# Performance work log

Measured on AMD Instinct MI355X. Metric: run time of the kernel, lower is better.

The kernel has to match this reference:

```python
import jax, jax.numpy as jnp
import numpy as np

D_HEAD = 64
IGNORE = -100000.0


def setup_inputs() -> dict:
    key = jax.random.key(0)
    ks = jax.random.split(key, 5)
    B, S, D, H, M = 2, 2048, 768, 12, D_HEAD
    scale = 0.05  # 'random_normal' keras init stddev
    return {
        "x": jax.random.normal(ks[0], (B, S, D), jnp.float32),
        "W_Q": jax.random.normal(ks[1], (H, D, M), jnp.float32) * scale,
        "b_Q": jnp.zeros((H, M), jnp.float32),
        "W_K": jax.random.normal(ks[2], (H, D, M), jnp.float32) * scale,
        "b_K": jnp.zeros((H, M), jnp.float32),
        "W_V": jax.random.normal(ks[3], (H, D, M), jnp.float32) * scale,
        "b_V": jnp.zeros((H, M), jnp.float32),
        "W_O": jax.random.normal(ks[4], (H, M, D), jnp.float32) * scale,
        "b_O": jnp.zeros((D,), jnp.float32),
    }


def reference(x, W_Q, b_Q, W_K, b_K, W_V, b_V, W_O, b_O):
    # q,k,v: [b, s, h, m]
    q = jnp.einsum("bqd,hdm->bqhm", x, W_Q) + b_Q
    k = jnp.einsum("bkd,hdm->bkhm", x, W_K) + b_K
    v = jnp.einsum("bkd,hdm->bkhm", x, W_V) + b_V
    # scores: [b, h, q, k], scaled by 1/sqrt(d_head)
    scores = jnp.einsum("bqhm,bkhm->bhqk", q, k) / jnp.sqrt(
        jnp.asarray(D_HEAD, q.dtype)
    )
    S = x.shape[1]
    # causal mask: strictly-upper-triangular positions set to IGNORE (-1e5),
    # matching tf.where(mask == 1, IGNORE, scores)
    causal = jnp.arange(S)[:, None] >= jnp.arange(S)[None, :]  # [q, k]
    scores = jnp.where(causal[None, None, :, :], scores, jnp.asarray(IGNORE, scores.dtype))
    pattern = jax.nn.softmax(scores, axis=-1)
    z = jnp.einsum("bhqk,bkhm->bqhm", pattern, v)
    attn_out = jnp.einsum("bqhm,hmd->bqd", z, W_O) + b_O
    return attn_out
```

## Files before the change

kernel.cpp:

```cpp
#include <hip/hip_runtime.h>
#include <hip/hip_bf16.h>
#include <cstdint>
#include <cstddef>

#define B_ 2
#define S_ 2048
#define D_ 768
#define H_ 12
#define M_ 64
#define BS_ (B_ * S_)
#define NQKV_ 2304
#define NCHUNK_ 80
#define TOTCHUNK_ (24 * NCHUNK_)
#define QSCALE 0.18033688011f

typedef __attribute__((ext_vector_type(8))) short bf16x8;
typedef __attribute__((ext_vector_type(4))) short bf16x4;
typedef __attribute__((ext_vector_type(4))) float f32x4;

__device__ __forceinline__ unsigned short f2bu(float f) {
    __hip_bfloat16 h = __float2bfloat16(f);
    unsigned short u;
    __builtin_memcpy(&u, &h, 2);
    return u;
}
__device__ __forceinline__ unsigned pack2(float a, float b) {
    return (unsigned)f2bu(a) | ((unsigned)f2bu(b) << 16);
}

__device__ __forceinline__ bf16x8 ld16(const unsigned short* p) {
    p = (const unsigned short*)__builtin_assume_aligned(p, 16);
    bf16x8 v; __builtin_memcpy(&v, p, 16); return v;
}
__device__ __forceinline__ bf16x4 ld8(const unsigned short* p) {
    p = (const unsigned short*)__builtin_assume_aligned(p, 8);
    bf16x4 v; __builtin_memcpy(&v, p, 8); return v;
}
__device__ __forceinline__ uint4 ld16u(const unsigned short* p) {
    p = (const unsigned short*)__builtin_assume_aligned(p, 16);
    uint4 v; __builtin_memcpy(&v, p, 16); return v;
}
__device__ __forceinline__ void st16(unsigned short* p, uint4 v) {
    p = (unsigned short*)__builtin_assume_aligned(p, 16);
    __builtin_memcpy(p, &v, 16);
}
__device__ __forceinline__ void st8(unsigned short* p, uint2 v) {
    p = (unsigned short*)__builtin_assume_aligned(p, 8);
    __builtin_memcpy(p, &v, 8);
}
__device__ __forceinline__ float4 ldf4(const float* p) {
    p = (const float*)__builtin_assume_aligned(p, 16);
    float4 v; __builtin_memcpy(&v, p, 16); return v;
}
__device__ __forceinline__ void async16(const unsigned short* g, unsigned short* l) {
    __builtin_amdgcn_global_load_lds(
        (const __attribute__((address_space(1))) void*)g,
        (__attribute__((address_space(3))) void*)l, 16, 0, 0);
}
__device__ __forceinline__ void b82f(uint4 u, float* o) {
    o[0] = __uint_as_float(u.x << 16); o[1] = __uint_as_float(u.x & 0xffff0000u);
    o[2] = __uint_as_float(u.y << 16); o[3] = __uint_as_float(u.y & 0xffff0000u);
    o[4] = __uint_as_float(u.z << 16); o[5] = __uint_as_float(u.z & 0xffff0000u);
    o[6] = __uint_as_float(u.w << 16); o[7] = __uint_as_float(u.w & 0xffff0000u);
}

#define NEG_BIG (-3.0e38f)

__global__ void prep(const float* __restrict__ WQ, const float* __restrict__ WK,
                     const float* __restrict__ WV, const float* __restrict__ WO,
                     const float* __restrict__ x,
                     unsigned short* __restrict__ WT,
                     unsigned short* __restrict__ WOT,
                     unsigned short* __restrict__ xb)
{
    const int bx = blockIdx.x;
    if (bx < 216) {
        const int xx = bx % 9, yy = bx / 9;
        const int c  = xx * 256 + threadIdx.x;
        const int k0 = yy * 32;
        const int which = c / D_;
        const int r = c - which * D_;
        const int h = r >> 6, m = r & 63;
        const float* Wsel = (which == 0) ? WQ : (which == 1) ? WK : WV;
        const float* src = Wsel + (size_t)h * D_ * M_ + m;
        unsigned short* dst = WT + (size_t)c * D_ + k0;
        for (int i = 0; i < 32; i += 8) {
            float wv[8];
#pragma unroll
            for (int j = 0; j < 8; j++) wv[j] = src[(size_t)(k0 + i + j) * M_];
            uint4 pu;
            pu.x = pack2(wv[0], wv[1]); pu.y = pack2(wv[2], wv[3]);
            pu.z = pack2(wv[4], wv[5]); pu.w = pack2(wv[6], wv[7]);
            st16(dst + i, pu);
        }
    } else if (bx < 288) {
        const int b2 = bx - 216;
        const int xx = b2 % 3, yy = b2 / 3;
        const int c  = xx * 256 + threadIdx.x;
        const int k0 = yy * 32;
        unsigned short* dst = WOT + (size_t)c * D_ + k0;
        for (int i = 0; i < 32; i += 8) {
            float wv[8];
#pragma unroll
            for (int j = 0; j < 8; j++) wv[j] = WO[(size_t)(k0 + i + j) * D_ + c];
            uint4 pu;
            pu.x = pack2(wv[0], wv[1]); pu.y = pack2(wv[2], wv[3]);
            pu.z = pack2(wv[4], wv[5]); pu.w = pack2(wv[6], wv[7]);
            st16(dst + i, pu);
        }
    } else {
        const size_t i = ((size_t)(bx - 288) * 256 + threadIdx.x) * 16;
#pragma unroll
        for (int p = 0; p < 2; p++) {
            float4 a0 = ldf4(x + i + p * 8), a1 = ldf4(x + i + p * 8 + 4);
            uint4 u;
            u.x = pack2(a0.x, a0.y); u.y = pack2(a0.z, a0.w);
            u.z = pack2(a1.x, a1.y); u.w = pack2(a1.z, a1.w);
            st16(xb + i + p * 8, u);
        }
    }
}

__global__ __launch_bounds__(256, 2) void qkv_gemm(
    const unsigned short* __restrict__ xb,
    const unsigned short* __restrict__ WT,
    const float* __restrict__ bQ, const float* __restrict__ bK,
    const float* __restrict__ bV,
    unsigned short* __restrict__ qo, unsigned short* __restrict__ ko,
    unsigned short* __restrict__ vt)
{
    const int row0 = blockIdx.x * 128;
    const int col0 = blockIdx.y * 128;
    const int t = threadIdx.x;
    const int w = t >> 6, lane = t & 63, quad = lane >> 4, l16 = lane & 15;
    const int wrow0 = (w & 1) * 64, wcol0 = (w >> 1) * 64;

    __shared__ unsigned short Alds[128 * 64];
    __shared__ unsigned short Blds[128 * 64];

    f32x4 acc[4][4] = {};

    const unsigned short* asrc[4];
    const unsigned short* bsrc[4];
    int ldsoff[4];
#pragma unroll
    for (int q = 0; q < 4; q++) {
        const int cq = w * 256 + q * 64 + lane;
        const int row = cq >> 3, c = cq & 7;
        const int cs = c ^ (row & 7);
        asrc[q] = xb + (size_t)(row0 + row) * D_ + cs * 8;
        bsrc[q] = WT + (size_t)(col0 + row) * D_ + cs * 8;
        ldsoff[q] = (w * 256 + q * 64) * 8;
    }
    const int swz = (l16 & 7);

    for (int k0 = 0; k0 < D_; k0 += 64) {
#pragma unroll
        for (int q = 0; q < 4; q++) async16(asrc[q] + k0, Alds + ldsoff[q]);
#pragma unroll
        for (int q = 0; q < 4; q++) async16(bsrc[q] + k0, Blds + ldsoff[q]);
        __syncthreads();

        bf16x8 af[4][2], bfm[4][2];
#pragma unroll
        for (int rt = 0; rt < 4; rt++) {
            const int row = wrow0 + rt * 16 + l16;
#pragma unroll
            for (int hh = 0; hh < 2; hh++)
                af[rt][hh] = ld16(&Alds[row * 64 + ((hh * 4 + quad) ^ swz) * 8]);
        }
#pragma unroll
        for (int st = 0; st < 4; st++) {
            const int row = wcol0 + st * 16 + l16;
#pragma unroll
            for (int hh = 0; hh < 2; hh++)
                bfm[st][hh] = ld16(&Blds[row * 64 + ((hh * 4 + quad) ^ swz) * 8]);
        }
#pragma unroll
        for (int rt = 0; rt < 4; rt++)
#pragma unroll
            for (int st = 0; st < 4; st++) {
                acc[rt][st] = __builtin_amdgcn_mfma_f32_16x16x32_bf16(
                    af[rt][0], bfm[st][0], acc[rt][st], 0, 0, 0);
                acc[rt][st] = __builtin_amdgcn_mfma_f32_16x16x32_bf16(
                    af[rt][1], bfm[st][1], acc[rt][st], 0, 0, 0);
            }
        __syncthreads();
    }

    const int which = col0 / D_;
    const int colin = col0 - which * D_;

    if (which < 2) {
        const float* bias = (which == 0) ? bQ : bK;
        unsigned short* outp = (which == 0) ? qo : ko;
        const float scale = (which == 0) ? QSCALE : 1.0f;
#pragma unroll
        for (int st = 0; st < 4; st++) {
            const int cl = colin + wcol0 + st * 16 + l16;
            const int h = cl >> 6, m = cl & 63;
            const float bval = bias[cl];
#pragma unroll
            for (int rt = 0; rt < 4; rt++)
#pragma unroll
                for (int rr = 0; rr < 4; rr++) {
                    const int R = row0 + wrow0 + rt * 16 + quad * 4 + rr;
                    const int bb = R >> 11, s = R & (S_ - 1);
                    outp[(((size_t)bb * H_ + h) * S_ + s) * M_ + m] =
                        f2bu((acc[rt][st][rr] + bval) * scale);
                }
        }
    } else {
#pragma unroll
        for (int st = 0; st < 4; st++) {
            const int cl = colin + wcol0 + st * 16 + l16;
            const int h = cl >> 6, m = cl & 63;
            const float bval = bV[cl];
#pragma unroll
            for (int rt = 0; rt < 4; rt++) {
                const int R0 = row0 + wrow0 + rt * 16 + quad * 4;
                const int bb = R0 >> 11, s0 = R0 & (S_ - 1);
                uint2 v;
                v.x = pack2(acc[rt][st][0] + bval, acc[rt][st][1] + bval);
                v.y = pack2(acc[rt][st][2] + bval, acc[rt][st][3] + bval);
                st8(&vt[(((size_t)bb * H_ + h) * M_ + m) * S_ + s0], v);
            }
        }
    }
}

struct StageRegs { uint4 ka[4]; uint4 va[4]; };

__device__ __forceinline__ void load_tile(const unsigned short* kb,
                                          const unsigned short* vb,
                                          int t, StageRegs& s)
{
#pragma unroll
    for (int q = 0; q < 4; q++) {
        const int ci = q * 256 + t;
        s.ka[q] = ld16u(kb + (size_t)(ci >> 3) * M_ + (ci & 7) * 8);
    }
#pragma unroll
    for (int q = 0; q < 4; q++) {
        const int ci = q * 256 + t;
        s.va[q] = ld16u(vb + (size_t)(ci >> 4) * S_ + (ci & 15) * 8);
    }
}

__global__ __launch_bounds__(256, 4) void attn_split(
    const unsigned short* __restrict__ Q,
    const unsigned short* __restrict__ Kin,
    const unsigned short* __restrict__ Vt,
    unsigned short* __restrict__ Opart,
    float* __restrict__ ml)
{
    const int xx = blockIdx.x;
    const int bh = blockIdx.y;

    int qt, c, nc;
    if (xx < 8)       { qt = xx; c = 0; nc = 1; }
    else if (xx < 24) { int u = xx - 8;  qt = 8  + (u >> 1); c = u & 1;  nc = 2; }
    else if (xx < 48) { int u = xx - 24; qt = 16 + u / 3;    c = u % 3;  nc = 3; }
    else              { int u = xx - 48; qt = 24 + (u >> 2); c = u & 3;  nc = 4; }

    const int ci     = bh * NCHUNK_ + xx;
    const int kbeg   = c * 512;
    const int keyend = min((qt + 1) * 64, kbeg + 512);
    const int iters  = (keyend - kbeg + 127) >> 7;
    const bool lastchunk = (c == nc - 1);

    const int t = threadIdx.x;
    const int wave = t >> 6, lane = t & 63, quad = lane >> 4, l16 = lane & 15;

    const unsigned short* Qb  = Q   + ((size_t)bh * S_ + qt * 64) * M_;
    const unsigned short* Kb  = Kin + (size_t)bh * S_ * M_;
    const unsigned short* VtB = Vt  + (size_t)bh * M_ * S_;

    __shared__ unsigned short Klds[128][72];
    __shared__ unsigned short Vlds[64][136];

    bf16x8 qf[2];
    {
        const unsigned short* qrow = Qb + (size_t)(wave * 16 + l16) * M_;
        qf[0] = ld16(qrow + quad * 8);
        qf[1] = ld16(qrow + 32 + quad * 8);
    }

    f32x4 o_acc[4] = {};
    float lrow = 0.f;

    StageRegs sr;
    load_tile(Kb + (size_t)kbeg * M_, VtB + kbeg, t, sr);

    for (int it = 0; it < iters; it++) {
        __syncthreads();
#pragma unroll
        for (int q = 0; q < 4; q++) {
            const int cq = q * 256 + t;
            st16(&Klds[cq >> 3][(cq & 7) * 8], sr.ka[q]);
        }
#pragma unroll
        for (int q = 0; q < 4; q++) {
            const int cq = q * 256 + t;
            st16(&Vlds[cq >> 4][(cq & 15) * 8], sr.va[q]);
        }
        __syncthreads();

        if (it + 1 < iters) {
            const int key1 = kbeg + (it + 1) * 128;
            load_tile(Kb + (size_t)key1 * M_, VtB + key1, t, sr);
        }

        f32x4 s_acc[8];
#pragma unroll
        for (int st = 0; st < 8; st++) {
            f32x4 z4 = {0.f, 0.f, 0.f, 0.f};
            bf16x8 kb0 = ld16(&Klds[st * 16 + l16][quad * 8]);
            bf16x8 kb1 = ld16(&Klds[st * 16 + l16][32 + quad * 8]);
            z4 = __builtin_amdgcn_mfma_f32_16x16x32_bf16(kb0, qf[0], z4, 0, 0, 0);
            z4 = __builtin_amdgcn_mfma_f32_16x16x32_bf16(kb1, qf[1], z4, 0, 0, 0);
            s_acc[st] = z4;
        }

        if (lastchunk && it == iters - 1) {
            const int keyq = kbeg + it * 128 + quad * 4;
            const int qg = qt * 64 + wave * 16 + l16;
#pragma unroll
            for (int st = 0; st < 8; st++)
#pragma unroll
                for (int r = 0; r < 4; r++)
                    if (keyq + st * 16 + r > qg)
                        s_acc[st][r] = -1e30f;
        }

        bf16x4 pkv[8];
#pragma unroll
        for (int st = 0; st < 8; st++) {
            float p0 = exp2f(s_acc[st][0]);
            float p1 = exp2f(s_acc[st][1]);
            float p2 = exp2f(s_acc[st][2]);
            float p3 = exp2f(s_acc[st][3]);
            lrow += (p0 + p1) + (p2 + p3);
            uint2 u;
            u.x = pack2(p0, p1);
            u.y = pack2(p2, p3);
            __builtin_memcpy(&pkv[st], &u, 8);
        }

#pragma unroll
        for (int stf = 0; stf < 4; stf++) {
#pragma unroll
            for (int st = 0; st < 8; st++) {
                bf16x4 va = ld8(&Vlds[stf * 16 + l16][st * 16 + quad * 4]);
                o_acc[stf] = __builtin_amdgcn_mfma_f32_16x16x16bf16_1k(
                    va, pkv[st], o_acc[stf], 0, 0, 0);
            }
        }
    }

    lrow += __shfl_xor(lrow, 16, 64);
    lrow += __shfl_xor(lrow, 32, 64);

    unsigned short* Op = Opart + (size_t)ci * 4096;
    const int q = wave * 16 + l16;
#pragma unroll
    for (int stf = 0; stf < 4; stf++) {
        uint2 u;
        u.x = pack2(o_acc[stf][0], o_acc[stf][1]);
        u.y = pack2(o_acc[stf][2], o_acc[stf][3]);
        st8(&Op[q * 64 + stf * 16 + quad * 4], u);
    }
    if (quad == 0)
        ml[(size_t)ci * 128 + 64 + q] = lrow;
}

__global__ void combine(const unsigned short* __restrict__ Opart,
                        const float* __restrict__ ml,
                        unsigned short* __restrict__ Z)
{
    const int qt = blockIdx.x, bh = blockIdx.y;
    const int b = bh / H_, h = bh - b * H_;
    const int g = qt >> 3, r7 = qt & 7;
    const int nc = g + 1;
    const int base = bh * NCHUNK_ + qt + 4 * g * (g - 1) + r7 * g;

    const int t = threadIdx.x;
    const int q = t >> 2, fs = (t & 3) * 16;

    float L = 0.f;
    for (int c = 0; c < nc; c++)
        L += ml[(size_t)(base + c) * 128 + 64 + q];
    const float invL = 1.0f / L;

    float o[16] = {};
    for (int c = 0; c < nc; c++) {
        const unsigned short* op =
            Opart + (size_t)(base + c) * 4096 + q * 64 + fs;
        float f[8];
        b82f(ld16u(op), f);
#pragma unroll
        for (int j = 0; j < 8; j++) o[j] += f[j];
        b82f(ld16u(op + 8), f);
#pragma unroll
        for (int j = 0; j < 8; j++) o[8 + j] += f[j];
    }

    unsigned short* zp =
        Z + ((size_t)b * S_ + qt * 64 + q) * (H_ * M_) + h * M_ + fs;
    uint4 u0, u1;
    u0.x = pack2(o[0]*invL,  o[1]*invL);  u0.y = pack2(o[2]*invL,  o[3]*invL);
    u0.z = pack2(o[4]*invL,  o[5]*invL);  u0.w = pack2(o[6]*invL,  o[7]*invL);
    u1.x = pack2(o[8]*invL,  o[9]*invL);  u1.y = pack2(o[10]*invL, o[11]*invL);
    u1.z = pack2(o[12]*invL, o[13]*invL); u1.w = pack2(o[14]*invL, o[15]*invL);
    st16(zp, u0);
    st16(zp + 8, u1);
}

__global__ __launch_bounds__(256, 2) void oproj_gemm(
    const unsigned short* __restrict__ Zin,
    const unsigned short* __restrict__ WOT,
    const float* __restrict__ bO,
    float* __restrict__ out)
{
    const int row0 = blockIdx.x * 128;
    const int col0 = blockIdx.y * 128;
    const int t = threadIdx.x;
    const int w = t >> 6, lane = t & 63, quad = lane >> 4, l16 = lane & 15;
    const int wrow0 = (w & 1) * 64, wcol0 = (w >> 1) * 64;

    __shared__ unsigned short Alds[128 * 64];
    __shared__ unsigned short Blds[128 * 64];

    f32x4 acc[4][4] = {};

    const unsigned short* asrc[4];
    const unsigned short* bsrc[4];
    int ldsoff[4];
#pragma unroll
    for (int q = 0; q < 4; q++) {
        const int cq = w * 256 + q * 64 + lane;
        const int row = cq >> 3, c = cq & 7;
        const int cs = c ^ (row & 7);
        asrc[q] = Zin + (size_t)(row0 + row) * D_ + cs * 8;
        bsrc[q] = WOT + (size_t)(col0 + row) * D_ + cs * 8;
        ldsoff[q] = (w * 256 + q * 64) * 8;
    }
    const int swz = (l16 & 7);

    for (int k0 = 0; k0 < D_; k0 += 64) {
#pragma unroll
        for (int q = 0; q < 4; q++) async16(asrc[q] + k0, Alds + ldsoff[q]);
#pragma unroll
        for (int q = 0; q < 4; q++) async16(bsrc[q] + k0, Blds + ldsoff[q]);
        __syncthreads();

        bf16x8 af[4][2], bfm[4][2];
#pragma unroll
        for (int rt = 0; rt < 4; rt++) {
            const int row = wrow0 + rt * 16 + l16;
#pragma unroll
            for (int hh = 0; hh < 2; hh++)
                af[rt][hh] = ld16(&Alds[row * 64 + ((hh * 4 + quad) ^ swz) * 8]);
        }
#pragma unroll
        for (int st = 0; st < 4; st++) {
            const int row = wcol0 + st * 16 + l16;
#pragma unroll
            for (int hh = 0; hh < 2; hh++)
                bfm[st][hh] = ld16(&Blds[row * 64 + ((hh * 4 + quad) ^ swz) * 8]);
        }
#pragma unroll
        for (int rt = 0; rt < 4; rt++)
#pragma unroll
            for (int st = 0; st < 4; st++) {
                acc[rt][st] = __builtin_amdgcn_mfma_f32_16x16x32_bf16(
                    af[rt][0], bfm[st][0], acc[rt][st], 0, 0, 0);
                acc[rt][st] = __builtin_amdgcn_mfma_f32_16x16x32_bf16(
                    af[rt][1], bfm[st][1], acc[rt][st], 0, 0, 0);
            }
        __syncthreads();
    }

#pragma unroll
    for (int st = 0; st < 4; st++) {
        const int c = col0 + wcol0 + st * 16 + l16;
        const float bval = bO[c];
#pragma unroll
        for (int rt = 0; rt < 4; rt++)
#pragma unroll
            for (int rr = 0; rr < 4; rr++) {
                const int R = row0 + wrow0 + rt * 16 + quad * 4 + rr;
                out[(size_t)R * D_ + c] = acc[rt][st][rr] + bval;
            }
    }
}

extern "C" void kernel_launch(void* const* d_in, const int* in_sizes, int n_in,
                              void* d_out, int out_size, void* d_ws, size_t ws_size,
                              hipStream_t stream)
{
    const float* x  = (const float*)d_in[0];
    const float* WQ = (const float*)d_in[1];
    const float* bQ = (const float*)d_in[2];
    const float* WK = (const float*)d_in[3];
    const float* bK = (const float*)d_in[4];
    const float* WV = (const float*)d_in[5];
    const float* bV = (const float*)d_in[6];
    const float* WO = (const float*)d_in[7];
    const float* bO = (const float*)d_in[8];
    float* out = (float*)d_out;

    const size_t n = (size_t)B_ * H_ * S_ * M_;
    unsigned short* q_ws  = (unsigned short*)d_ws;
    unsigned short* k_ws  = q_ws + n;
    unsigned short* vt_ws = k_ws + n;
    unsigned short* z_ws  = vt_ws + n;
    unsigned short* WT    = z_ws + n;
    unsigned short* WOT   = WT + (size_t)NQKV_ * D_;
    unsigned short* xb    = WOT + (size_t)D_ * D_;
    unsigned short* Opart = xb + (size_t)BS_ * D_;
    float* mlbuf = (float*)(Opart + (size_t)TOTCHUNK_ * 4096);

    prep<<<dim3(1056), 256, 0, stream>>>(WQ, WK, WV, WO, x, WT, WOT, xb);
    qkv_gemm<<<dim3(BS_ / 128, NQKV_ / 128), 256, 0, stream>>>(
        xb, WT, bQ, bK, bV, q_ws, k_ws, vt_ws);
    attn_split<<<dim3(NCHUNK_, B_ * H_), 256, 0, stream>>>(
        q_ws, k_ws, vt_ws, Opart, mlbuf);
    combine<<<dim3(S_ / 64, B_ * H_), 256, 0, stream>>>(Opart, mlbuf, z_ws);
    oproj_gemm<<<dim3(BS_ / 128, D_ / 128), 256, 0, stream>>>(
        z_ws, WOT, bO, out);
}
```

Baseline: 164.4 us.

## Swizzle K/V shared-memory layout, reorder attention blocks heaviest-first, raise occupancy

Drops the padded K and V shared-memory tiles in favour of unpadded, XOR-swizzled layouts. This lowers LDS usage while still avoiding bank conflicts on the MFMA operand reads. It also remaps the block index so the longest causal chunks launch first and heads interleave, and raises the launch-bounds occupancy hint from 4 to 5 blocks. The swizzle adds per-lane index arithmetic and an 8-entry offset array, which could push up register pressure under the tighter occupancy target.

```diff
diff --git a/kernel.cpp b/kernel.cpp
--- a/kernel.cpp
+++ b/kernel.cpp
@@ -247,15 +247,16 @@
     }
 }
 
-__global__ __launch_bounds__(256, 4) void attn_split(
+__global__ __launch_bounds__(256, 5) void attn_split(
     const unsigned short* __restrict__ Q,
     const unsigned short* __restrict__ Kin,
     const unsigned short* __restrict__ Vt,
     unsigned short* __restrict__ Opart,
     float* __restrict__ ml)
 {
-    const int xx = blockIdx.x;
-    const int bh = blockIdx.y;
+    const int flat = blockIdx.y * NCHUNK_ + blockIdx.x;
+    const int bh = flat % 24;
+    const int xx = (NCHUNK_ - 1) - flat / 24;
 
     int qt, c, nc;
     if (xx < 8)       { qt = xx; c = 0; nc = 1; }
@@ -276,8 +277,8 @@
     const unsigned short* Kb  = Kin + (size_t)bh * S_ * M_;
     const unsigned short* VtB = Vt  + (size_t)bh * M_ * S_;
 
-    __shared__ unsigned short Klds[128][72];
-    __shared__ unsigned short Vlds[64][136];
+    __shared__ unsigned short Klds[128 * 64];
+    __shared__ unsigned short Vlds[64 * 128];
 
     bf16x8 qf[2];
     {
@@ -286,6 +287,15 @@
         qf[1] = ld16(qrow + 32 + quad * 8);
     }
 
+    const int ksw = l16 & 7;
+    const int ko0 = (quad ^ ksw) * 8;
+    const int ko1 = ((quad + 4) ^ ksw) * 8;
+    int voff[8];
+#pragma unroll
+    for (int st = 0; st < 8; st++)
+        voff[st] = l16 * 128 + (quad ^ (l16 & 3)) * 4
+                 + ((st ^ ((l16 >> 2) & 3)) << 4);
+
     f32x4 o_acc[4] = {};
     float lrow = 0.f;
 
@@ -297,12 +307,21 @@
 #pragma unroll
         for (int q = 0; q < 4; q++) {
             const int cq = q * 256 + t;
-            st16(&Klds[cq >> 3][(cq & 7) * 8], sr.ka[q]);
+            const int row = cq >> 3;
+            const int bp = (cq & 7) ^ (row & 7);
+            st16(&Klds[row * 64 + bp * 8], sr.ka[q]);
         }
 #pragma unroll
         for (int q = 0; q < 4; q++) {
             const int cq = q * 256 + t;
-            st16(&Vlds[cq >> 4][(cq & 15) * 8], sr.va[q]);
+            const int f = cq >> 4, pl = cq & 15;
+            const int pp = pl ^ ((f >> 1) & 7);
+            uint4 v = sr.va[q];
+            if (f & 1) {
+                unsigned tx = v.x, ty = v.y;
+                v.x = v.z; v.y = v.w; v.z = tx; v.w = ty;
+            }
+            st16(&Vlds[f * 128 + pp * 8], v);
         }
         __syncthreads();
 
@@ -315,10 +334,11 @@
 #pragma unroll
         for (int st = 0; st < 8; st++) {
             f32x4 z4 = {0.f, 0.f, 0.f, 0.f};
-            bf16x8 kb0 = ld16(&Klds[st * 16 + l16][quad * 8]);
-            bf16x8 kb1 = ld16(&Klds[st * 16 + l16][32 + quad * 8]);
-            z4 = __builtin_amdgcn_mfma_f32_16x16x32_bf16(kb0, qf[0], z4, 0, 0, 0);
-            z4 = __builtin_amdgcn_mfma_f32_16x16x32_bf16(kb1, qf[1], z4, 0, 0, 0);
+            const unsigned short* krow = &Klds[(st * 16 + l16) * 64];
+            bf16x8 k0 = ld16(krow + ko0);
+            bf16x8 k1 = ld16(krow + ko1);
+            z4 = __builtin_amdgcn_mfma_f32_16x16x32_bf16(k0, qf[0], z4, 0, 0, 0);
+            z4 = __builtin_amdgcn_mfma_f32_16x16x32_bf16(k1, qf[1], z4, 0, 0, 0);
             s_acc[st] = z4;
         }
 
@@ -351,7 +371,7 @@
         for (int stf = 0; stf < 4; stf++) {
 #pragma unroll
             for (int st = 0; st < 8; st++) {
-                bf16x4 va = ld8(&Vlds[stf * 16 + l16][st * 16 + quad * 4]);
+                bf16x4 va = ld8(&Vlds[stf * 2048 + voff[st]]);
                 o_acc[stf] = __builtin_amdgcn_mfma_f32_16x16x16bf16_1k(
                     va, pkv[st], o_acc[stf], 0, 0, 0);
             }
```

Result: slower. 235.8 us (+43.4%).
